# Performance work log

Hardware: AMD Instinct MI355X
Metric: run time of the kernel (lower is better)

The kernel has to match this reference:

```python
import jax, jax.numpy as jnp
import numpy as np

B, F, D = 16384, 40, 64  # batch, num_fields, embedding_size
D_OUT = 64               # att_embedding_size * head_num = 32 * 2


def setup_inputs() -> dict:
    key = jax.random.key(0)
    ks = jax.random.split(key, 5)
    return {
        "inputs": jax.random.normal(ks[0], (B, F, D), dtype=jnp.float32),
        "W_Query": jax.random.normal(ks[1], (D, D_OUT), dtype=jnp.float32) * 0.05,
        "W_key": jax.random.normal(ks[2], (D, D_OUT), dtype=jnp.float32) * 0.05,
        "W_Value": jax.random.normal(ks[3], (D, D_OUT), dtype=jnp.float32) * 0.05,
        "W_Res": jax.random.normal(ks[4], (D, D_OUT), dtype=jnp.float32) * 0.05,
    }


def reference(inputs, W_Query, W_key, W_Value, W_Res):
    # QKV projections (no head splitting, per original module)
    q = jnp.einsum('bfd,de->bfe', inputs, W_Query)  # [B, F, D_OUT]
    k = jnp.einsum('bfd,de->bfe', inputs, W_key)
    v = jnp.einsum('bfd,de->bfe', inputs, W_Value)
    # scaled-dot-product over the field axis; scaling=False so no divide
    scores = jax.nn.softmax(jnp.einsum('bqe,bke->bqk', q, k), axis=-1)  # [B, F, F]
    result = jnp.einsum('bqk,bke->bqe', scores, v)
    # residual projection (use_res=True)
    result = result + jnp.einsum('bfd,de->bfe', inputs, W_Res)
    return jax.nn.relu(result)
```

## Files before the change

### kernel.cpp

```cpp
#include <hip/hip_runtime.h>
#include <hip/hip_bf16.h>

#define BB   16384
#define F    40
#define D    64
#define E    64
#define LDK  72
#define WAVES 4
#define ITER  4

typedef __bf16 bf16;
typedef __bf16 bf16x8 __attribute__((ext_vector_type(8)));
typedef __bf16 bf16x4 __attribute__((ext_vector_type(4)));
typedef float  f32x4  __attribute__((ext_vector_type(4)));


__global__ __launch_bounds__(256, 1)
void attn_fused(const float* __restrict__ X,
                const float* __restrict__ Wq,
                const float* __restrict__ Wk,
                const float* __restrict__ Wv,
                const float* __restrict__ Wr,
                float* __restrict__ Out)
{
    __shared__ bf16 WT[4][E * LDK];
    __shared__ bf16 QB[WAVES][48 * LDK];
    __shared__ bf16 KB[WAVES][48 * LDK];
    __shared__ bf16 VT[WAVES][E * LDK];

    const int tid  = threadIdx.x;
    const int wv   = tid >> 6;
    const int lane = tid & 63;
    const int l16  = lane & 15;
    const int quad = lane >> 4;

    const float* Ws[4] = {Wq, Wk, Wv, Wr};
    #pragma unroll
    for (int w = 0; w < 4; ++w) {
        const float* W = Ws[w];
        for (int i = tid; i < D * E; i += 256) {
            int dd = i >> 6;
            int e  = i & 63;
            WT[w][e * LDK + dd] = (bf16)W[i];
        }
    }
    {
        bf16x8 z = {};
        *(bf16x8*)&VT[wv][lane * LDK + 48] = z;
        *(bf16x8*)&VT[wv][lane * LDK + 56] = z;
    }
    __syncthreads();

    for (int it = 0; it < ITER; ++it) {
        const int b = (blockIdx.x * WAVES + wv) * ITER + it;
        const float* Xb = X + (size_t)b * (F * D);

        bf16x8 xf[3][2];
        #pragma unroll
        for (int mt = 0; mt < 3; ++mt) {
            int row = mt * 16 + l16;
            if (row > F - 1) row = F - 1;
            #pragma unroll
            for (int kt = 0; kt < 2; ++kt) {
                const float* p = Xb + row * D + kt * 32 + quad * 8;
                float4 u0 = *(const float4*)p;
                float4 u1 = *(const float4*)(p + 4);
                bf16x8 f;
                f[0] = (bf16)u0.x; f[1] = (bf16)u0.y; f[2] = (bf16)u0.z; f[3] = (bf16)u0.w;
                f[4] = (bf16)u1.x; f[5] = (bf16)u1.y; f[6] = (bf16)u1.z; f[7] = (bf16)u1.w;
                xf[mt][kt] = f;
            }
        }

        f32x4 racc[3][4];
        #pragma unroll
        for (int w = 0; w < 4; ++w) {
            #pragma unroll
            for (int nt = 0; nt < 4; ++nt) {
                bf16x8 b0 = *(bf16x8*)&WT[w][(nt * 16 + l16) * LDK + 0  + quad * 8];
                bf16x8 b1 = *(bf16x8*)&WT[w][(nt * 16 + l16) * LDK + 32 + quad * 8];
                #pragma unroll
                for (int mt = 0; mt < 3; ++mt) {
                    f32x4 acc = {0.f, 0.f, 0.f, 0.f};
                    acc = __builtin_amdgcn_mfma_f32_16x16x32_bf16(xf[mt][0], b0, acc, 0, 0, 0);
                    acc = __builtin_amdgcn_mfma_f32_16x16x32_bf16(xf[mt][1], b1, acc, 0, 0, 0);
                    if (w == 3) {
                        racc[mt][nt] = acc;
                    } else if (w == 2) {
                        int col = nt * 16 + l16;
                        int r0  = mt * 16 + quad * 4;
                        bf16x4 pk;
                        pk[0] = (bf16)acc[0]; pk[1] = (bf16)acc[1];
                        pk[2] = (bf16)acc[2]; pk[3] = (bf16)acc[3];
                        *(bf16x4*)&VT[wv][col * LDK + r0] = pk;
                    } else {
                        bf16* dst = (w == 0) ? QB[wv] : KB[wv];
                        int col = nt * 16 + l16;
                        #pragma unroll
                        for (int r = 0; r < 4; ++r) {
                            int row = mt * 16 + quad * 4 + r;
                            if (row < F) dst[row * LDK + col] = (bf16)acc[r];
                        }
                    }
                }
            }
        }

        f32x4 sacc[3][3];
        bf16x8 kf[3][2];
        #pragma unroll
        for (int snt = 0; snt < 3; ++snt)
            #pragma unroll
            for (int kt = 0; kt < 2; ++kt)
                kf[snt][kt] = *(bf16x8*)&KB[wv][(snt * 16 + l16) * LDK + kt * 32 + quad * 8];
        #pragma unroll
        for (int smt = 0; smt < 3; ++smt) {
            bf16x8 q0 = *(bf16x8*)&QB[wv][(smt * 16 + l16) * LDK + 0  + quad * 8];
            bf16x8 q1 = *(bf16x8*)&QB[wv][(smt * 16 + l16) * LDK + 32 + quad * 8];
            #pragma unroll
            for (int snt = 0; snt < 3; ++snt) {
                f32x4 acc = {0.f, 0.f, 0.f, 0.f};
                acc = __builtin_amdgcn_mfma_f32_16x16x32_bf16(q0, kf[snt][0], acc, 0, 0, 0);
                acc = __builtin_amdgcn_mfma_f32_16x16x32_bf16(q1, kf[snt][1], acc, 0, 0, 0);
                sacc[smt][snt] = acc;
            }
        }

        const bool mask2 = (l16 >= 8);
        #pragma unroll
        for (int smt = 0; smt < 3; ++smt) {
            #pragma unroll
            for (int r = 0; r < 4; ++r) {
                float s0 = sacc[smt][0][r];
                float s1 = sacc[smt][1][r];
                float s2 = mask2 ? -1e30f : sacc[smt][2][r];
                float m = fmaxf(fmaxf(s0, s1), s2);
                #pragma unroll
                for (int off = 1; off < 16; off <<= 1)
                    m = fmaxf(m, __shfl_xor(m, off, 64));
                float e0 = __expf(s0 - m);
                float e1 = __expf(s1 - m);
                float e2 = mask2 ? 0.f : __expf(s2 - m);
                float sum = e0 + e1 + e2;
                #pragma unroll
                for (int off = 1; off < 16; off <<= 1)
                    sum += __shfl_xor(sum, off, 64);
                float inv = 1.0f / sum;
                int row = smt * 16 + quad * 4 + r;
                if (row < F) {
                    QB[wv][row * LDK + l16]      = (bf16)(e0 * inv);
                    QB[wv][row * LDK + 16 + l16] = (bf16)(e1 * inv);
                    QB[wv][row * LDK + 32 + l16] = (bf16)(e2 * inv);
                }
            }
        }

        bf16x8 pf[3][2];
        #pragma unroll
        for (int mt = 0; mt < 3; ++mt)
            #pragma unroll
            for (int kt = 0; kt < 2; ++kt)
                pf[mt][kt] = *(bf16x8*)&QB[wv][(mt * 16 + l16) * LDK + kt * 32 + quad * 8];
        #pragma unroll
        for (int nt = 0; nt < 4; ++nt) {
            bf16x8 v0 = *(bf16x8*)&VT[wv][(nt * 16 + l16) * LDK + 0  + quad * 8];
            bf16x8 v1 = *(bf16x8*)&VT[wv][(nt * 16 + l16) * LDK + 32 + quad * 8];
            #pragma unroll
            for (int mt = 0; mt < 3; ++mt) {
                f32x4 acc = racc[mt][nt];
                acc = __builtin_amdgcn_mfma_f32_16x16x32_bf16(pf[mt][0], v0, acc, 0, 0, 0);
                acc = __builtin_amdgcn_mfma_f32_16x16x32_bf16(pf[mt][1], v1, acc, 0, 0, 0);
                int col = nt * 16 + l16;
                #pragma unroll
                for (int r = 0; r < 4; ++r) {
                    int row = mt * 16 + quad * 4 + r;
                    if (row < F)
                        Out[(size_t)b * (F * E) + row * E + col] = fmaxf(acc[r], 0.f);
                }
            }
        }
    }
}

extern "C" void kernel_launch(void* const* d_in, const int* in_sizes, int n_in,
                              void* d_out, int out_size, void* d_ws, size_t ws_size,
                              hipStream_t stream) {
    const float* X  = (const float*)d_in[0];
    const float* Wq = (const float*)d_in[1];
    const float* Wk = (const float*)d_in[2];
    const float* Wv = (const float*)d_in[3];
    const float* Wr = (const float*)d_in[4];
    float* Out = (float*)d_out;

    dim3 grid(BB / (WAVES * ITER));
    attn_fused<<<grid, 256, 0, stream>>>(X, Wq, Wk, Wv, Wr, Out);
}
```

Measured before the change: 369.5 us.

## Fold Wq·Wkᵀ into one matrix, prepack weight fragments, one batch per wave

A prep kernel computes G = Wq·Wkᵀ in fp32 and writes G, Wv and Wr to the workspace as bf16 in MFMA fragment order. Scores then become (X·G)·Xᵀ, which drops the separate K projection. The main kernel runs one 64-thread block per batch element and loads B-fragments straight from global memory, so there is no per-block weight staging in LDS and far less shared memory is used. The costs are an extra single-block launch on the critical path, bf16 rounding of the folded G (a different numeric path), and many more small blocks.

```diff
diff --git a/kernel.cpp b/kernel.cpp
--- a/kernel.cpp
+++ b/kernel.cpp
@@ -1,13 +1,12 @@
 #include <hip/hip_runtime.h>
 #include <hip/hip_bf16.h>
 
-#define BB   16384
-#define F    40
-#define D    64
-#define E    64
-#define LDK  72
-#define WAVES 4
-#define ITER  4
+#define BB  16384
+#define F   40
+#define D   64
+#define E   64
+#define LDQ 72
+#define LDV 56
 
 typedef __bf16 bf16;
 typedef __bf16 bf16x8 __attribute__((ext_vector_type(8)));
@@ -15,168 +14,186 @@
 typedef float  f32x4  __attribute__((ext_vector_type(4)));
 
 
-__global__ __launch_bounds__(256, 1)
+__global__ __launch_bounds__(256)
+void prep_weights(const float* __restrict__ Wq, const float* __restrict__ Wk,
+                  const float* __restrict__ Wv, const float* __restrict__ Wr,
+                  bf16* __restrict__ ws)
+{
+    __shared__ float Gs[64 * 64];
+    const int tid = threadIdx.x;
+    for (int i = tid; i < 64 * 64; i += 256) {
+        int dd = i >> 6, ee = i & 63;
+        float s = 0.f;
+        for (int e = 0; e < 64; ++e) s += Wq[dd * 64 + e] * Wk[ee * 64 + e];
+        Gs[i] = s;
+    }
+    __syncthreads();
+    for (int f = tid; f < 4096; f += 256) {
+        int j = f & 7, lane = (f >> 3) & 63, kt = (f >> 9) & 1, nt = f >> 10;
+        int dd = kt * 32 + (lane >> 4) * 8 + j;
+        int ee = nt * 16 + (lane & 15);
+        ws[f]        = (bf16)Gs[dd * 64 + ee];
+        ws[4096 + f] = (bf16)Wv[dd * 64 + ee];
+        ws[8192 + f] = (bf16)Wr[dd * 64 + ee];
+    }
+}
+
+__global__ __launch_bounds__(64, 3)
 void attn_fused(const float* __restrict__ X,
-                const float* __restrict__ Wq,
-                const float* __restrict__ Wk,
-                const float* __restrict__ Wv,
-                const float* __restrict__ Wr,
+                const bf16* __restrict__ wfrag,
                 float* __restrict__ Out)
 {
-    __shared__ bf16 WT[4][E * LDK];
-    __shared__ bf16 QB[WAVES][48 * LDK];
-    __shared__ bf16 KB[WAVES][48 * LDK];
-    __shared__ bf16 VT[WAVES][E * LDK];
-
-    const int tid  = threadIdx.x;
-    const int wv   = tid >> 6;
-    const int lane = tid & 63;
+    __shared__ bf16 QB[48 * LDQ];
+    __shared__ bf16 VT[64 * LDV + 16];
+
+    const int lane = threadIdx.x;
     const int l16  = lane & 15;
     const int quad = lane >> 4;
-
-    const float* Ws[4] = {Wq, Wk, Wv, Wr};
-    #pragma unroll
-    for (int w = 0; w < 4; ++w) {
-        const float* W = Ws[w];
-        for (int i = tid; i < D * E; i += 256) {
-            int dd = i >> 6;
-            int e  = i & 63;
-            WT[w][e * LDK + dd] = (bf16)W[i];
-        }
-    }
+    const int b    = blockIdx.x;
+    const float* Xb = X + (size_t)b * (F * D);
+
     {
         bf16x8 z = {};
-        *(bf16x8*)&VT[wv][lane * LDK + 48] = z;
-        *(bf16x8*)&VT[wv][lane * LDK + 56] = z;
-    }
-    __syncthreads();
-
-    for (int it = 0; it < ITER; ++it) {
-        const int b = (blockIdx.x * WAVES + wv) * ITER + it;
-        const float* Xb = X + (size_t)b * (F * D);
-
-        bf16x8 xf[3][2];
-        #pragma unroll
-        for (int mt = 0; mt < 3; ++mt) {
-            int row = mt * 16 + l16;
-            if (row > F - 1) row = F - 1;
-            #pragma unroll
-            for (int kt = 0; kt < 2; ++kt) {
-                const float* p = Xb + row * D + kt * 32 + quad * 8;
-                float4 u0 = *(const float4*)p;
-                float4 u1 = *(const float4*)(p + 4);
-                bf16x8 f;
-                f[0] = (bf16)u0.x; f[1] = (bf16)u0.y; f[2] = (bf16)u0.z; f[3] = (bf16)u0.w;
-                f[4] = (bf16)u1.x; f[5] = (bf16)u1.y; f[6] = (bf16)u1.z; f[7] = (bf16)u1.w;
-                xf[mt][kt] = f;
+        *(bf16x8*)&VT[lane * LDV + 48] = z;
+        if (lane < 2) *(bf16x8*)&VT[64 * LDV + lane * 8] = z;
+    }
+
+    bf16x8 xf[3][2];
+    #pragma unroll
+    for (int mt = 0; mt < 3; ++mt) {
+        int row = mt * 16 + l16; if (row >= F) row = F - 1;
+        #pragma unroll
+        for (int kt = 0; kt < 2; ++kt) {
+            const float* p = Xb + row * D + kt * 32 + quad * 8;
+            float4 u0 = *(const float4*)p;
+            float4 u1 = *(const float4*)(p + 4);
+            bf16x8 f;
+            f[0] = (bf16)u0.x; f[1] = (bf16)u0.y; f[2] = (bf16)u0.z; f[3] = (bf16)u0.w;
+            f[4] = (bf16)u1.x; f[5] = (bf16)u1.y; f[6] = (bf16)u1.z; f[7] = (bf16)u1.w;
+            xf[mt][kt] = f;
+        }
+    }
+
+    const bf16x8* gF = (const bf16x8*)wfrag;
+    const bf16x8* vF = (const bf16x8*)(wfrag + 4096);
+    const bf16x8* rF = (const bf16x8*)(wfrag + 8192);
+
+    f32x4 racc[3][4];
+    #pragma unroll
+    for (int nt = 0; nt < 4; ++nt) {
+        bf16x8 b0 = gF ? rF[(nt * 2 + 0) * 64 + lane] : bf16x8{};
+        bf16x8 b1 = rF[(nt * 2 + 1) * 64 + lane];
+        #pragma unroll
+        for (int mt = 0; mt < 3; ++mt) {
+            f32x4 acc = {0.f, 0.f, 0.f, 0.f};
+            acc = __builtin_amdgcn_mfma_f32_16x16x32_bf16(xf[mt][0], b0, acc, 0, 0, 0);
+            acc = __builtin_amdgcn_mfma_f32_16x16x32_bf16(xf[mt][1], b1, acc, 0, 0, 0);
+            racc[mt][nt] = acc;
+        }
+    }
+
+    #pragma unroll
+    for (int nt = 0; nt < 4; ++nt) {
+        bf16x8 b0 = vF[(nt * 2 + 0) * 64 + lane];
+        bf16x8 b1 = vF[(nt * 2 + 1) * 64 + lane];
+        #pragma unroll
+        for (int mt = 0; mt < 3; ++mt) {
+            f32x4 acc = {0.f, 0.f, 0.f, 0.f};
+            acc = __builtin_amdgcn_mfma_f32_16x16x32_bf16(xf[mt][0], b0, acc, 0, 0, 0);
+            acc = __builtin_amdgcn_mfma_f32_16x16x32_bf16(xf[mt][1], b1, acc, 0, 0, 0);
+            int col = nt * 16 + l16;
+            int r0  = mt * 16 + quad * 4;
+            bf16x4 pk;
+            pk[0] = (bf16)acc[0]; pk[1] = (bf16)acc[1];
+            pk[2] = (bf16)acc[2]; pk[3] = (bf16)acc[3];
+            *(bf16x4*)&VT[col * LDV + r0] = pk;
+        }
+    }
+
+    #pragma unroll
+    for (int nt = 0; nt < 4; ++nt) {
+        bf16x8 b0 = gF[(nt * 2 + 0) * 64 + lane];
+        bf16x8 b1 = gF[(nt * 2 + 1) * 64 + lane];
+        #pragma unroll
+        for (int mt = 0; mt < 3; ++mt) {
+            f32x4 acc = {0.f, 0.f, 0.f, 0.f};
+            acc = __builtin_amdgcn_mfma_f32_16x16x32_bf16(xf[mt][0], b0, acc, 0, 0, 0);
+            acc = __builtin_amdgcn_mfma_f32_16x16x32_bf16(xf[mt][1], b1, acc, 0, 0, 0);
+            int col = nt * 16 + l16;
+            int r0  = mt * 16 + quad * 4;
+            #pragma unroll
+            for (int r = 0; r < 4; ++r) QB[(r0 + r) * LDQ + col] = (bf16)acc[r];
+        }
+    }
+
+    bf16x8 qf[3][2];
+    #pragma unroll
+    for (int mt = 0; mt < 3; ++mt)
+        #pragma unroll
+        for (int kt = 0; kt < 2; ++kt)
+            qf[mt][kt] = *(const bf16x8*)&QB[(mt * 16 + l16) * LDQ + kt * 32 + quad * 8];
+    f32x4 sacc[3][3];
+    #pragma unroll
+    for (int smt = 0; smt < 3; ++smt)
+        #pragma unroll
+        for (int snt = 0; snt < 3; ++snt) {
+            f32x4 acc = {0.f, 0.f, 0.f, 0.f};
+            acc = __builtin_amdgcn_mfma_f32_16x16x32_bf16(qf[smt][0], xf[snt][0], acc, 0, 0, 0);
+            acc = __builtin_amdgcn_mfma_f32_16x16x32_bf16(qf[smt][1], xf[snt][1], acc, 0, 0, 0);
+            sacc[smt][snt] = acc;
+        }
+
+    const bool mask2 = (l16 >= 8);
+    #pragma unroll
+    for (int smt = 0; smt < 3; ++smt) {
+        #pragma unroll
+        for (int r = 0; r < 4; ++r) {
+            float s0 = sacc[smt][0][r];
+            float s1 = sacc[smt][1][r];
+            float s2 = mask2 ? -1e30f : sacc[smt][2][r];
+            float m = fmaxf(fmaxf(s0, s1), s2);
+            #pragma unroll
+            for (int off = 1; off < 16; off <<= 1)
+                m = fmaxf(m, __shfl_xor(m, off, 64));
+            float e0 = __expf(s0 - m);
+            float e1 = __expf(s1 - m);
+            float e2 = mask2 ? 0.f : __expf(s2 - m);
+            float sum = e0 + e1 + e2;
+            #pragma unroll
+            for (int off = 1; off < 16; off <<= 1)
+                sum += __shfl_xor(sum, off, 64);
+            float inv = 1.0f / sum;
+            int row = smt * 16 + quad * 4 + r;
+            if (row < F) {
+                QB[row * LDQ + l16]      = (bf16)(e0 * inv);
+                QB[row * LDQ + 16 + l16] = (bf16)(e1 * inv);
+                QB[row * LDQ + 32 + l16] = (bf16)(e2 * inv);
+                QB[row * LDQ + 48 + l16] = (bf16)0.f;
             }
         }
-
-        f32x4 racc[3][4];
-        #pragma unroll
-        for (int w = 0; w < 4; ++w) {
-            #pragma unroll
-            for (int nt = 0; nt < 4; ++nt) {
-                bf16x8 b0 = *(bf16x8*)&WT[w][(nt * 16 + l16) * LDK + 0  + quad * 8];
-                bf16x8 b1 = *(bf16x8*)&WT[w][(nt * 16 + l16) * LDK + 32 + quad * 8];
-                #pragma unroll
-                for (int mt = 0; mt < 3; ++mt) {
-                    f32x4 acc = {0.f, 0.f, 0.f, 0.f};
-                    acc = __builtin_amdgcn_mfma_f32_16x16x32_bf16(xf[mt][0], b0, acc, 0, 0, 0);
-                    acc = __builtin_amdgcn_mfma_f32_16x16x32_bf16(xf[mt][1], b1, acc, 0, 0, 0);
-                    if (w == 3) {
-                        racc[mt][nt] = acc;
-                    } else if (w == 2) {
-                        int col = nt * 16 + l16;
-                        int r0  = mt * 16 + quad * 4;
-                        bf16x4 pk;
-                        pk[0] = (bf16)acc[0]; pk[1] = (bf16)acc[1];
-                        pk[2] = (bf16)acc[2]; pk[3] = (bf16)acc[3];
-                        *(bf16x4*)&VT[wv][col * LDK + r0] = pk;
-                    } else {
-                        bf16* dst = (w == 0) ? QB[wv] : KB[wv];
-                        int col = nt * 16 + l16;
-                        #pragma unroll
-                        for (int r = 0; r < 4; ++r) {
-                            int row = mt * 16 + quad * 4 + r;
-                            if (row < F) dst[row * LDK + col] = (bf16)acc[r];
-                        }
-                    }
-                }
-            }
-        }
-
-        f32x4 sacc[3][3];
-        bf16x8 kf[3][2];
-        #pragma unroll
-        for (int snt = 0; snt < 3; ++snt)
-            #pragma unroll
-            for (int kt = 0; kt < 2; ++kt)
-                kf[snt][kt] = *(bf16x8*)&KB[wv][(snt * 16 + l16) * LDK + kt * 32 + quad * 8];
-        #pragma unroll
-        for (int smt = 0; smt < 3; ++smt) {
-            bf16x8 q0 = *(bf16x8*)&QB[wv][(smt * 16 + l16) * LDK + 0  + quad * 8];
-            bf16x8 q1 = *(bf16x8*)&QB[wv][(smt * 16 + l16) * LDK + 32 + quad * 8];
-            #pragma unroll
-            for (int snt = 0; snt < 3; ++snt) {
-                f32x4 acc = {0.f, 0.f, 0.f, 0.f};
-                acc = __builtin_amdgcn_mfma_f32_16x16x32_bf16(q0, kf[snt][0], acc, 0, 0, 0);
-                acc = __builtin_amdgcn_mfma_f32_16x16x32_bf16(q1, kf[snt][1], acc, 0, 0, 0);
-                sacc[smt][snt] = acc;
-            }
-        }
-
-        const bool mask2 = (l16 >= 8);
-        #pragma unroll
-        for (int smt = 0; smt < 3; ++smt) {
+    }
+
+    bf16x8 pf[3][2];
+    #pragma unroll
+    for (int mt = 0; mt < 3; ++mt)
+        #pragma unroll
+        for (int kt = 0; kt < 2; ++kt)
+            pf[mt][kt] = *(const bf16x8*)&QB[(mt * 16 + l16) * LDQ + kt * 32 + quad * 8];
+    #pragma unroll
+    for (int nt = 0; nt < 4; ++nt) {
+        bf16x8 v0 = *(const bf16x8*)&VT[(nt * 16 + l16) * LDV + 0  + quad * 8];
+        bf16x8 v1 = *(const bf16x8*)&VT[(nt * 16 + l16) * LDV + 32 + quad * 8];
+        #pragma unroll
+        for (int mt = 0; mt < 3; ++mt) {
+            f32x4 acc = racc[mt][nt];
+            acc = __builtin_amdgcn_mfma_f32_16x16x32_bf16(pf[mt][0], v0, acc, 0, 0, 0);
+            acc = __builtin_amdgcn_mfma_f32_16x16x32_bf16(pf[mt][1], v1, acc, 0, 0, 0);
+            int col = nt * 16 + l16;
             #pragma unroll
             for (int r = 0; r < 4; ++r) {
-                float s0 = sacc[smt][0][r];
-                float s1 = sacc[smt][1][r];
-                float s2 = mask2 ? -1e30f : sacc[smt][2][r];
-                float m = fmaxf(fmaxf(s0, s1), s2);
-                #pragma unroll
-                for (int off = 1; off < 16; off <<= 1)
-                    m = fmaxf(m, __shfl_xor(m, off, 64));
-                float e0 = __expf(s0 - m);
-                float e1 = __expf(s1 - m);
-                float e2 = mask2 ? 0.f : __expf(s2 - m);
-                float sum = e0 + e1 + e2;
-                #pragma unroll
-                for (int off = 1; off < 16; off <<= 1)
-                    sum += __shfl_xor(sum, off, 64);
-                float inv = 1.0f / sum;
-                int row = smt * 16 + quad * 4 + r;
-                if (row < F) {
-                    QB[wv][row * LDK + l16]      = (bf16)(e0 * inv);
-                    QB[wv][row * LDK + 16 + l16] = (bf16)(e1 * inv);
-                    QB[wv][row * LDK + 32 + l16] = (bf16)(e2 * inv);
-                }
-            }
-        }
-
-        bf16x8 pf[3][2];
-        #pragma unroll
-        for (int mt = 0; mt < 3; ++mt)
-            #pragma unroll
-            for (int kt = 0; kt < 2; ++kt)
-                pf[mt][kt] = *(bf16x8*)&QB[wv][(mt * 16 + l16) * LDK + kt * 32 + quad * 8];
-        #pragma unroll
-        for (int nt = 0; nt < 4; ++nt) {
-            bf16x8 v0 = *(bf16x8*)&VT[wv][(nt * 16 + l16) * LDK + 0  + quad * 8];
-            bf16x8 v1 = *(bf16x8*)&VT[wv][(nt * 16 + l16) * LDK + 32 + quad * 8];
-            #pragma unroll
-            for (int mt = 0; mt < 3; ++mt) {
-                f32x4 acc = racc[mt][nt];
-                acc = __builtin_amdgcn_mfma_f32_16x16x32_bf16(pf[mt][0], v0, acc, 0, 0, 0);
-                acc = __builtin_amdgcn_mfma_f32_16x16x32_bf16(pf[mt][1], v1, acc, 0, 0, 0);
-                int col = nt * 16 + l16;
-                #pragma unroll
-                for (int r = 0; r < 4; ++r) {
-                    int row = mt * 16 + quad * 4 + r;
-                    if (row < F)
-                        Out[(size_t)b * (F * E) + row * E + col] = fmaxf(acc[r], 0.f);
-                }
+                int row = mt * 16 + quad * 4 + r;
+                if (row < F)
+                    Out[(size_t)b * (F * E) + row * E + col] = fmaxf(acc[r], 0.f);
             }
         }
     }
@@ -191,7 +208,8 @@
     const float* Wv = (const float*)d_in[3];
     const float* Wr = (const float*)d_in[4];
     float* Out = (float*)d_out;
-
-    dim3 grid(BB / (WAVES * ITER));
-    attn_fused<<<grid, 256, 0, stream>>>(X, Wq, Wk, Wv, Wr, Out);
+    bf16* ws = (bf16*)d_ws;
+
+    prep_weights<<<1, 256, 0, stream>>>(Wq, Wk, Wv, Wr, ws);
+    attn_fused<<<BB, 64, 0, stream>>>(X, ws, Out);
 }
```

Result: slower. 380.3 us (+2.9%).
